# Optimization experiments

Measured on AMD Instinct MI355X. Metric: run time of the kernel, lower is better.

Reference implementation:

```python
import jax, jax.numpy as jnp
import numpy as np

E, MAX_M, K, N = 8, 2048, 2048, 8192

def setup_inputs() -> dict:
    key = jax.random.key(0)
    k1, k2, k3 = jax.random.split(key, 3)
    x_padded = jax.random.normal(k1, (E, MAX_M, K), dtype=jnp.float32)
    stacked_weights = jax.random.normal(k2, (E, N, K), dtype=jnp.float32) * 0.02
    m_sizes = jax.random.randint(k3, (E,), 0, MAX_M, dtype=jnp.int32)
    return {"x_padded": x_padded, "stacked_weights": stacked_weights, "m_sizes": m_sizes}

def reference(x_padded, stacked_weights, m_sizes):
    # valid-token mask per expert: [E, MAX_M]
    mask = (jnp.arange(MAX_M, dtype=jnp.int32)[None, :] < m_sizes[:, None])
    # zero padded rows (pad_expert_inputs fills with zeros)
    x = jnp.where(mask[:, :, None], x_padded, jnp.zeros((), x_padded.dtype))
    # grouped GEMM via batched matmul: [E, M, K] x [E, N, K]^T -> [E, M, N]
    out = jnp.einsum('emk,enk->emn', x, stacked_weights)
    # rows beyond m_sizes[i] are sliced away in the original; mask them to zero
    return jnp.where(mask[:, :, None], out, jnp.zeros((), out.dtype))
```

## Files before the change

kernel.cpp:

```cpp
#include <hip/hip_runtime.h>
#include <hip/hip_bf16.h>


#define NE   8
#define MAXM 2048
#define KD   2048
#define ND   8192

#define BM   256
#define BN   256
#define BK   64
#define NTS  (KD/BK)

typedef __attribute__((ext_vector_type(8))) short          short8;
typedef __attribute__((ext_vector_type(8))) unsigned short us8;
typedef __attribute__((ext_vector_type(4))) float          f32x4;
typedef __attribute__((ext_vector_type(4))) unsigned short us4;

__device__ __forceinline__ unsigned short f2bf(float f) {
    union { float f; unsigned u; } v; v.f = f;
    unsigned u = v.u;
    return (unsigned short)((u + 0x7FFFu + ((u >> 16) & 1u)) >> 16);
}

__device__ __forceinline__ void gload16(const void* g, void* l) {
    __builtin_amdgcn_global_load_lds(
        (const __attribute__((address_space(1))) void*)g,
        (__attribute__((address_space(3))) void*)l, 16, 0, 0);
}

__global__ __launch_bounds__(256) void cvt_kernel(const float* __restrict__ src,
                                                  unsigned short* __restrict__ dst,
                                                  int n8) {
    int i = blockIdx.x * blockDim.x + threadIdx.x;
    int stride = gridDim.x * blockDim.x;
    for (; i < n8; i += stride) {
        const f32x4* s = (const f32x4*)(src + (size_t)i * 8);
        f32x4 a = s[0], b = s[1];
        us8 v = (us8){f2bf(a[0]), f2bf(a[1]), f2bf(a[2]), f2bf(a[3]),
                      f2bf(b[0]), f2bf(b[1]), f2bf(b[2]), f2bf(b[3])};
        *(us8*)(dst + (size_t)i * 8) = v;
    }
}

__global__ __launch_bounds__(256) void cvt_x_kernel(const float* __restrict__ src,
                                                    unsigned short* __restrict__ dst,
                                                    const int* __restrict__ ms) {
    int bid = blockIdx.x;
    int e = bid >> 11, m = bid & 2047;
    if (m >= ms[e]) return;
    const float* s = src + ((size_t)e * MAXM + m) * KD;
    unsigned short* d = dst + ((size_t)e * MAXM + m) * KD;
    int t = threadIdx.x;
    const f32x4* s4 = (const f32x4*)(s + t * 8);
    f32x4 a = s4[0], b = s4[1];
    us8 v = (us8){f2bf(a[0]), f2bf(a[1]), f2bf(a[2]), f2bf(a[3]),
                  f2bf(b[0]), f2bf(b[1]), f2bf(b[2]), f2bf(b[3])};
    *(us8*)(d + t * 8) = v;
}

__global__ __launch_bounds__(512, 2) void ggemm_pers(
    const unsigned short* __restrict__ xb,
    const unsigned short* __restrict__ wb,
    const int*   __restrict__ ms,
    float*       __restrict__ out)
{
    int p   = blockIdx.x;
    int xcd = p & 7;
    int jj  = p >> 3;
    int tid = threadIdx.x;

    __shared__ int s_live[8], s_dead[8], s_cnt[2];
    __shared__ unsigned short Ak[2][2][BM * 32];
    __shared__ unsigned short Bk[2][2][BN * 32];

    if (tid == 0) {
        int nl = 0, nd = 0, cumL = 0, cumD = 0, il = jj, id = jj;
        #pragma unroll
        for (int e = 0; e < NE; ++e) {
            int L = (ms[e] + 255) >> 8;
            int cntL = L << 2, cntD = (8 - L) << 2;
            while (il < cumL + cntL) { int o = il - cumL; s_live[nl++] = (e << 5) | ((o >> 2) << 2) | (o & 3); il += 32; }
            while (id < cumD + cntD) { int o = id - cumD; s_dead[nd++] = (e << 5) | ((L + (o >> 2)) << 2) | (o & 3); id += 32; }
            cumL += cntL; cumD += cntD;
        }
        s_cnt[0] = nl; s_cnt[1] = nd;
    }
    __syncthreads();

    int ndead = s_cnt[1];
    #pragma unroll 1
    for (int d = 0; d < ndead; ++d) {
        int v = s_dead[d]; int e = v >> 5, br = (v >> 2) & 7, bcl = v & 3;
        float* outE = out + (size_t)e * MAXM * ND;
        int row0 = br * BM, col0 = (xcd * 4 + bcl) * BN;
        f32x4 z = (f32x4){0.f, 0.f, 0.f, 0.f};
        #pragma unroll
        for (int q = 0; q < 32; ++q) {
            int i2 = tid + q * 512;
            int rr = i2 >> 6, cc = (i2 & 63) << 2;
            *(f32x4*)(outE + (size_t)(row0 + rr) * ND + col0 + cc) = z;
        }
    }
    int nlive = s_cnt[0];
    if (nlive == 0) return;

    int wid = tid >> 6, lane = tid & 63;
    int wr = wid >> 2, wc = wid & 3;
    int lr = lane & 15, kg = lane >> 4;
    int srow = lane >> 2;
    int ss   = (lane & 3) ^ ((lane >> 3) & 3);

    auto stageA = [&](int b, int kh, const unsigned short* xP, int kt) {
        #pragma unroll
        for (int q = 0; q < 2; ++q) {
            int blk = wid * 2 + q;
            const unsigned short* src =
                xP + (size_t)(blk * 16 + srow) * KD + kt * BK + kh * 32 + ss * 8;
            gload16(src, (char*)&Ak[b][kh][0] + blk * 1024);
        }
    };
    auto stageB = [&](int b, int kh, const unsigned short* wP, int kt) {
        #pragma unroll
        for (int q = 0; q < 2; ++q) {
            int blk = wid * 2 + q;
            const unsigned short* src =
                wP + (size_t)(blk * 16 + srow) * KD + kt * BK + kh * 32 + ss * 8;
            gload16(src, (char*)&Bk[b][kh][0] + blk * 1024);
        }
    };
    auto ldA = [&](short8* a, int b, int kh) {
        #pragma unroll
        for (int mf = 0; mf < 8; ++mf) {
            int row  = wr * 128 + mf * 16 + lr;
            int slot = kg ^ ((row >> 1) & 3);
            a[mf] = *(const short8*)&Ak[b][kh][row * 32 + slot * 8];
        }
    };
    auto ldB4 = [&](short8* bf, int b, int kh) {
        #pragma unroll
        for (int i = 0; i < 4; ++i) {
            int row  = wc * 64 + i * 16 + lr;
            int slot = kg ^ ((row >> 1) & 3);
            bf[i] = *(const short8*)&Bk[b][kh][row * 32 + slot * 8];
        }
    };

    f32x4 acc[8][4];
    #pragma unroll
    for (int mf = 0; mf < 8; ++mf)
        #pragma unroll
        for (int nf = 0; nf < 4; ++nf)
            acc[mf][nf] = (f32x4){0.f, 0.f, 0.f, 0.f};

    const unsigned short *xC, *wC, *xN, *wN;
    float *oC, *oN;
    int msC, r0C, c0C, msN, r0N, c0N;
    {
        int v = s_live[0]; int e = v >> 5, br = (v >> 2) & 7, bcl = v & 3;
        r0C = br * BM; c0C = (xcd * 4 + bcl) * BN; msC = ms[e];
        xC = xb + ((size_t)e * MAXM + r0C) * KD;
        wC = wb + ((size_t)e * ND + c0C) * KD;
        oC = out + (size_t)e * MAXM * ND;
    }
    if (nlive > 1) {
        int v = s_live[1]; int e = v >> 5, br = (v >> 2) & 7, bcl = v & 3;
        r0N = br * BM; c0N = (xcd * 4 + bcl) * BN; msN = ms[e];
        xN = xb + ((size_t)e * MAXM + r0N) * KD;
        wN = wb + ((size_t)e * ND + c0N) * KD;
        oN = out + (size_t)e * MAXM * ND;
    } else { xN = xC; wN = wC; oN = oC; msN = msC; r0N = r0C; c0N = c0C; }

    stageA(0, 0, xC, 0); stageB(0, 0, wC, 0);
    stageA(0, 1, xC, 0); stageB(0, 1, wC, 0);
    stageA(1, 0, xC, 1); stageB(1, 0, wC, 1);
    asm volatile("s_waitcnt vmcnt(8)" ::: "memory");
    __builtin_amdgcn_s_barrier();

    #pragma unroll 1
    for (int s = 0; s < nlive; ++s) {
        bool last  = (s + 1 >= nlive);
        bool alive = (r0C + wr * 128) < msC;

        auto tile = [&](int b, int kt) {
            bool g1 = (kt + 1 < NTS) || (!last);
            bool g2 = (kt + 2 < NTS) || (!last);
            const unsigned short* xS1 = (kt + 1 < NTS) ? xC : xN;
            const unsigned short* wS1 = (kt + 1 < NTS) ? wC : wN;
            int k1 = (kt + 1 < NTS) ? kt + 1 : 0;
            const unsigned short* xS2 = (kt + 2 < NTS) ? xC : xN;
            const unsigned short* wS2 = (kt + 2 < NTS) ? wC : wN;
            int k2 = (kt + 2 < NTS) ? kt + 2 : kt + 2 - NTS;

            short8 a[8], bf[4];
            if (alive) { ldA(a, b, 0); ldB4(bf, b, 0); }
            if (g1) { stageA(b ^ 1, 1, xS1, k1); stageB(b ^ 1, 1, wS1, k1); }
            __builtin_amdgcn_s_barrier();
            __builtin_amdgcn_s_setprio(1);
            if (alive) {
                #pragma unroll
                for (int mf = 0; mf < 8; ++mf)
                    #pragma unroll
                    for (int nf = 0; nf < 4; ++nf)
                        acc[mf][nf] = __builtin_amdgcn_mfma_f32_16x16x32_bf16(a[mf], bf[nf], acc[mf][nf], 0, 0, 0);
            }
            __builtin_amdgcn_s_setprio(0);
            if (g1) { asm volatile("s_waitcnt vmcnt(8)" ::: "memory"); }
            else    { asm volatile("s_waitcnt vmcnt(0)" ::: "memory"); }
            __builtin_amdgcn_s_barrier();
            if (alive) { ldA(a, b, 1); ldB4(bf, b, 1); }
            if (g2) { stageA(b, 0, xS2, k2); stageB(b, 0, wS2, k2); }
            __builtin_amdgcn_s_barrier();
            __builtin_amdgcn_s_setprio(1);
            if (alive) {
                #pragma unroll
                for (int mf = 0; mf < 8; ++mf)
                    #pragma unroll
                    for (int nf = 0; nf < 4; ++nf)
                        acc[mf][nf] = __builtin_amdgcn_mfma_f32_16x16x32_bf16(a[mf], bf[nf], acc[mf][nf], 0, 0, 0);
            }
            __builtin_amdgcn_s_setprio(0);
            if (g2) { asm volatile("s_waitcnt vmcnt(8)" ::: "memory"); }
            else    { asm volatile("s_waitcnt vmcnt(0)" ::: "memory"); }
            __builtin_amdgcn_s_barrier();
        };

        #pragma unroll 1
        for (int kt = 0; kt < NTS; kt += 2) {
            tile(0, kt);
            tile(1, kt + 1);
        }

        #pragma unroll
        for (int mf = 0; mf < 8; ++mf) {
            int rbase = r0C + wr * 128 + mf * 16 + kg * 4;
            #pragma unroll
            for (int nf = 0; nf < 4; ++nf) {
                int gc = c0C + wc * 64 + nf * 16 + lr;
                #pragma unroll
                for (int q = 0; q < 4; ++q) {
                    int gr = rbase + q;
                    float v = (gr < msC) ? acc[mf][nf][q] : 0.f;
                    oC[(size_t)gr * ND + gc] = v;
                    acc[mf][nf][q] = 0.f;
                }
            }
        }

        xC = xN; wC = wN; oC = oN; msC = msN; r0C = r0N; c0C = c0N;
        if (s + 2 < nlive) {
            int v = s_live[s + 2]; int e = v >> 5, br = (v >> 2) & 7, bcl = v & 3;
            r0N = br * BM; c0N = (xcd * 4 + bcl) * BN; msN = ms[e];
            xN = xb + ((size_t)e * MAXM + r0N) * KD;
            wN = wb + ((size_t)e * ND + c0N) * KD;
            oN = out + (size_t)e * MAXM * ND;
        }
    }
}

#define FBM 128
#define FBK 32
#define FTM (MAXM/FBM)
#define FTN (ND/FBM)
#define FNT (KD/FBK)
#define LSTR 40
__global__ __launch_bounds__(256, 2) void ggemm_fused(
    const float* __restrict__ x, const float* __restrict__ w,
    const int* __restrict__ ms, float* __restrict__ out)
{
    int nwg  = gridDim.x;
    int orig = blockIdx.x;
    int cpx  = nwg >> 3;
    int bid  = (orig & 7) * cpx + (orig >> 3);
    int e   = bid / (FTM * FTN);
    int rem = bid % (FTM * FTN);
    int br  = rem % FTM;
    int bc  = rem / FTM;
    int m_size = ms[e];
    int row0 = br * FBM, col0 = bc * FBM;
    float* outE = out + (size_t)e * MAXM * ND;
    int tid = threadIdx.x;

    if (row0 >= m_size) {
        f32x4 z = (f32x4){0.f, 0.f, 0.f, 0.f};
        #pragma unroll
        for (int q = 0; q < 16; ++q) {
            int i2 = tid + q * 256;
            int rr = i2 >> 5, cc = (i2 & 31) << 2;
            *(f32x4*)(outE + (size_t)(row0 + rr) * ND + col0 + cc) = z;
        }
        return;
    }

    const float* xE = x + ((size_t)e * MAXM + row0) * KD;
    const float* wE = w + ((size_t)e * ND   + col0) * KD;

    __shared__ unsigned short As[2][FBM][LSTR];
    __shared__ unsigned short Bs[2][FBM][LSTR];

    int sr  = tid >> 3;
    int sc4 = tid & 7;
    int wid = tid >> 6, lane = tid & 63;
    int wr = wid >> 1, wc = wid & 1;
    int lr = lane & 15, kg = lane >> 4;

    f32x4 acc[4][4];
    #pragma unroll
    for (int m = 0; m < 4; ++m)
        #pragma unroll
        for (int n = 0; n < 4; ++n)
            acc[m][n] = (f32x4){0.f, 0.f, 0.f, 0.f};

    {
        #pragma unroll
        for (int q = 0; q < 4; ++q) {
            int r0 = sr + q * 32;
            f32x4 av = *(const f32x4*)(xE + (size_t)r0 * KD + sc4 * 4);
            f32x4 bv = *(const f32x4*)(wE + (size_t)r0 * KD + sc4 * 4);
            us4 ah = (us4){f2bf(av[0]), f2bf(av[1]), f2bf(av[2]), f2bf(av[3])};
            us4 bh = (us4){f2bf(bv[0]), f2bf(bv[1]), f2bf(bv[2]), f2bf(bv[3])};
            *(us4*)&As[0][r0][sc4 * 4] = ah;
            *(us4*)&Bs[0][r0][sc4 * 4] = bh;
        }
    }
    __syncthreads();

    for (int t = 0; t < FNT; ++t) {
        int cur = t & 1;
        f32x4 av[4], bv[4];
        bool pre = (t + 1 < FNT);
        if (pre) {
            const float* xk = xE + (size_t)(t + 1) * FBK;
            const float* wk = wE + (size_t)(t + 1) * FBK;
            #pragma unroll
            for (int q = 0; q < 4; ++q) {
                int r0 = sr + q * 32;
                av[q] = *(const f32x4*)(xk + (size_t)r0 * KD + sc4 * 4);
                bv[q] = *(const f32x4*)(wk + (size_t)r0 * KD + sc4 * 4);
            }
        }
        short8 a[4], b[4];
        #pragma unroll
        for (int m = 0; m < 4; ++m)
            a[m] = *(const short8*)&As[cur][wr * 64 + m * 16 + lr][kg * 8];
        #pragma unroll
        for (int n = 0; n < 4; ++n)
            b[n] = *(const short8*)&Bs[cur][wc * 64 + n * 16 + lr][kg * 8];
        #pragma unroll
        for (int m = 0; m < 4; ++m)
            #pragma unroll
            for (int n = 0; n < 4; ++n)
                acc[m][n] = __builtin_amdgcn_mfma_f32_16x16x32_bf16(a[m], b[n], acc[m][n], 0, 0, 0);

        if (pre) {
            int nb = cur ^ 1;
            #pragma unroll
            for (int q = 0; q < 4; ++q) {
                int r0 = sr + q * 32;
                us4 ah = (us4){f2bf(av[q][0]), f2bf(av[q][1]), f2bf(av[q][2]), f2bf(av[q][3])};
                us4 bh = (us4){f2bf(bv[q][0]), f2bf(bv[q][1]), f2bf(bv[q][2]), f2bf(bv[q][3])};
                *(us4*)&As[nb][r0][sc4 * 4] = ah;
                *(us4*)&Bs[nb][r0][sc4 * 4] = bh;
            }
        }
        __syncthreads();
    }

    #pragma unroll
    for (int m = 0; m < 4; ++m) {
        int rbase = row0 + wr * 64 + m * 16 + kg * 4;
        #pragma unroll
        for (int n = 0; n < 4; ++n) {
            int gc = col0 + wc * 64 + n * 16 + lr;
            #pragma unroll
            for (int q = 0; q < 4; ++q) {
                int gr = rbase + q;
                float v = (gr < m_size) ? acc[m][n][q] : 0.f;
                outE[(size_t)gr * ND + gc] = v;
            }
        }
    }
}

extern "C" void kernel_launch(void* const* d_in, const int* in_sizes, int n_in,
                              void* d_out, int out_size, void* d_ws, size_t ws_size,
                              hipStream_t stream) {
    const float* x  = (const float*)d_in[0];
    const float* w  = (const float*)d_in[1];
    const int*   ms = (const int*)d_in[2];
    float* out = (float*)d_out;

    const size_t xElems = (size_t)NE * MAXM * KD;
    const size_t wElems = (size_t)NE * ND   * KD;
    const size_t need   = (xElems + wElems) * 2;

    if (ws_size >= need) {
        unsigned short* xb = (unsigned short*)d_ws;
        unsigned short* wb = xb + xElems;
        cvt_x_kernel<<<NE * MAXM, 256, 0, stream>>>(x, xb, ms);
        cvt_kernel<<<2048, 256, 0, stream>>>(w, wb, (int)(wElems / 8));
        ggemm_pers<<<256, 512, 0, stream>>>(xb, wb, ms, out);
    } else {
        ggemm_fused<<<dim3(NE * (MAXM/FBM) * (ND/FBM)), dim3(256), 0, stream>>>(x, w, ms, out);
    }
}
```

Before: 581.2 us.

## Restructure GEMM K-loop pipeline to one barrier per half-tile phase

```diff
diff --git a/kernel.cpp b/kernel.cpp
--- a/kernel.cpp
+++ b/kernel.cpp
@@ -129,22 +129,6 @@
             gload16(src, (char*)&Bk[b][kh][0] + blk * 1024);
         }
     };
-    auto ldA = [&](short8* a, int b, int kh) {
-        #pragma unroll
-        for (int mf = 0; mf < 8; ++mf) {
-            int row  = wr * 128 + mf * 16 + lr;
-            int slot = kg ^ ((row >> 1) & 3);
-            a[mf] = *(const short8*)&Ak[b][kh][row * 32 + slot * 8];
-        }
-    };
-    auto ldB4 = [&](short8* bf, int b, int kh) {
-        #pragma unroll
-        for (int i = 0; i < 4; ++i) {
-            int row  = wc * 64 + i * 16 + lr;
-            int slot = kg ^ ((row >> 1) & 3);
-            bf[i] = *(const short8*)&Bk[b][kh][row * 32 + slot * 8];
-        }
-    };
 
     f32x4 acc[8][4];
     #pragma unroll
@@ -173,62 +157,49 @@
 
     stageA(0, 0, xC, 0); stageB(0, 0, wC, 0);
     stageA(0, 1, xC, 0); stageB(0, 1, wC, 0);
-    stageA(1, 0, xC, 1); stageB(1, 0, wC, 1);
-    asm volatile("s_waitcnt vmcnt(8)" ::: "memory");
-    __builtin_amdgcn_s_barrier();
 
     #pragma unroll 1
     for (int s = 0; s < nlive; ++s) {
         bool last  = (s + 1 >= nlive);
         bool alive = (r0C + wr * 128) < msC;
 
-        auto tile = [&](int b, int kt) {
-            bool g1 = (kt + 1 < NTS) || (!last);
-            bool g2 = (kt + 2 < NTS) || (!last);
-            const unsigned short* xS1 = (kt + 1 < NTS) ? xC : xN;
-            const unsigned short* wS1 = (kt + 1 < NTS) ? wC : wN;
-            int k1 = (kt + 1 < NTS) ? kt + 1 : 0;
-            const unsigned short* xS2 = (kt + 2 < NTS) ? xC : xN;
-            const unsigned short* wS2 = (kt + 2 < NTS) ? wC : wN;
-            int k2 = (kt + 2 < NTS) ? kt + 2 : kt + 2 - NTS;
-
-            short8 a[8], bf[4];
-            if (alive) { ldA(a, b, 0); ldB4(bf, b, 0); }
-            if (g1) { stageA(b ^ 1, 1, xS1, k1); stageB(b ^ 1, 1, wS1, k1); }
+        auto phase = [&](int b, int kh, bool vm4, bool stg,
+                         const unsigned short* xS, const unsigned short* wS, int kts) {
+            if (vm4) { asm volatile("s_waitcnt vmcnt(4)" ::: "memory"); }
+            else     { asm volatile("s_waitcnt vmcnt(0)" ::: "memory"); }
             __builtin_amdgcn_s_barrier();
-            __builtin_amdgcn_s_setprio(1);
+            if (stg) { stageA(b ^ 1, kh, xS, kts); stageB(b ^ 1, kh, wS, kts); }
             if (alive) {
+                short8 a[8], bf[4];
+                #pragma unroll
+                for (int i = 0; i < 4; ++i) {
+                    int row  = wc * 64 + i * 16 + lr;
+                    int slot = kg ^ ((row >> 1) & 3);
+                    bf[i] = *(const short8*)&Bk[b][kh][row * 32 + slot * 8];
+                }
+                #pragma unroll
+                for (int mf = 0; mf < 8; ++mf) {
+                    int row  = wr * 128 + mf * 16 + lr;
+                    int slot = kg ^ ((row >> 1) & 3);
+                    a[mf] = *(const short8*)&Ak[b][kh][row * 32 + slot * 8];
+                }
                 #pragma unroll
                 for (int mf = 0; mf < 8; ++mf)
                     #pragma unroll
                     for (int nf = 0; nf < 4; ++nf)
                         acc[mf][nf] = __builtin_amdgcn_mfma_f32_16x16x32_bf16(a[mf], bf[nf], acc[mf][nf], 0, 0, 0);
             }
-            __builtin_amdgcn_s_setprio(0);
-            if (g1) { asm volatile("s_waitcnt vmcnt(8)" ::: "memory"); }
-            else    { asm volatile("s_waitcnt vmcnt(0)" ::: "memory"); }
-            __builtin_amdgcn_s_barrier();
-            if (alive) { ldA(a, b, 1); ldB4(bf, b, 1); }
-            if (g2) { stageA(b, 0, xS2, k2); stageB(b, 0, wS2, k2); }
-            __builtin_amdgcn_s_barrier();
-            __builtin_amdgcn_s_setprio(1);
-            if (alive) {
-                #pragma unroll
-                for (int mf = 0; mf < 8; ++mf)
-                    #pragma unroll
-                    for (int nf = 0; nf < 4; ++nf)
-                        acc[mf][nf] = __builtin_amdgcn_mfma_f32_16x16x32_bf16(a[mf], bf[nf], acc[mf][nf], 0, 0, 0);
-            }
-            __builtin_amdgcn_s_setprio(0);
-            if (g2) { asm volatile("s_waitcnt vmcnt(8)" ::: "memory"); }
-            else    { asm volatile("s_waitcnt vmcnt(0)" ::: "memory"); }
-            __builtin_amdgcn_s_barrier();
         };
 
         #pragma unroll 1
-        for (int kt = 0; kt < NTS; kt += 2) {
-            tile(0, kt);
-            tile(1, kt + 1);
+        for (int kt = 0; kt < NTS; ++kt) {
+            int b = kt & 1;
+            bool has_next = (kt + 1 < NTS) || (!last);
+            const unsigned short* xS = (kt + 1 < NTS) ? xC : xN;
+            const unsigned short* wS = (kt + 1 < NTS) ? wC : wN;
+            int kts = (kt + 1 < NTS) ? kt + 1 : 0;
+            phase(b, 0, true, has_next, xS, wS, kts);
+            phase(b, 1, has_next, has_next, xS, wS, kts);
         }
 
         #pragma unroll
```

Measured after the change: 663.1 us. 1.14x slower.

## Fuse fp32-to-bf16 weight conversion into persistent GEMM B-tile staging

Applied to the files above, without the earlier changes.

```diff
diff --git a/kernel.cpp b/kernel.cpp
--- a/kernel.cpp
+++ b/kernel.cpp
@@ -27,20 +27,6 @@
     __builtin_amdgcn_global_load_lds(
         (const __attribute__((address_space(1))) void*)g,
         (__attribute__((address_space(3))) void*)l, 16, 0, 0);
-}
-
-__global__ __launch_bounds__(256) void cvt_kernel(const float* __restrict__ src,
-                                                  unsigned short* __restrict__ dst,
-                                                  int n8) {
-    int i = blockIdx.x * blockDim.x + threadIdx.x;
-    int stride = gridDim.x * blockDim.x;
-    for (; i < n8; i += stride) {
-        const f32x4* s = (const f32x4*)(src + (size_t)i * 8);
-        f32x4 a = s[0], b = s[1];
-        us8 v = (us8){f2bf(a[0]), f2bf(a[1]), f2bf(a[2]), f2bf(a[3]),
-                      f2bf(b[0]), f2bf(b[1]), f2bf(b[2]), f2bf(b[3])};
-        *(us8*)(dst + (size_t)i * 8) = v;
-    }
 }
 
 __global__ __launch_bounds__(256) void cvt_x_kernel(const float* __restrict__ src,
@@ -61,7 +47,7 @@
 
 __global__ __launch_bounds__(512, 2) void ggemm_pers(
     const unsigned short* __restrict__ xb,
-    const unsigned short* __restrict__ wb,
+    const float*          __restrict__ w,
     const int*   __restrict__ ms,
     float*       __restrict__ out)
 {
@@ -108,8 +94,10 @@
     int wid = tid >> 6, lane = tid & 63;
     int wr = wid >> 2, wc = wid & 3;
     int lr = lane & 15, kg = lane >> 4;
-    int srow = lane >> 2;
-    int ss   = (lane & 3) ^ ((lane >> 3) & 3);
+    int srow  = lane >> 2;
+    int ss    = (lane & 3) ^ ((lane >> 3) & 3);
+    int sslot = lane & 3;
+    int ssw   = sslot ^ ((lane >> 3) & 3);
 
     auto stageA = [&](int b, int kh, const unsigned short* xP, int kt) {
         #pragma unroll
@@ -120,13 +108,23 @@
             gload16(src, (char*)&Ak[b][kh][0] + blk * 1024);
         }
     };
-    auto stageB = [&](int b, int kh, const unsigned short* wP, int kt) {
+    auto loadB = [&](f32x4* bl, const float* wP, int kt, int kh) {
         #pragma unroll
         for (int q = 0; q < 2; ++q) {
             int blk = wid * 2 + q;
-            const unsigned short* src =
-                wP + (size_t)(blk * 16 + srow) * KD + kt * BK + kh * 32 + ss * 8;
-            gload16(src, (char*)&Bk[b][kh][0] + blk * 1024);
+            const float* src = wP + (size_t)(blk * 16 + srow) * KD + kt * BK + kh * 32 + sslot * 8;
+            bl[2 * q]     = *(const f32x4*)(src);
+            bl[2 * q + 1] = *(const f32x4*)(src + 4);
+        }
+    };
+    auto writeB = [&](int b, int kh, const f32x4* bl) {
+        #pragma unroll
+        for (int q = 0; q < 2; ++q) {
+            int blk = wid * 2 + q;
+            f32x4 lo = bl[2 * q], hi = bl[2 * q + 1];
+            us8 v = (us8){f2bf(lo[0]), f2bf(lo[1]), f2bf(lo[2]), f2bf(lo[3]),
+                          f2bf(hi[0]), f2bf(hi[1]), f2bf(hi[2]), f2bf(hi[3])};
+            *(us8*)((char*)&Bk[b][kh][0] + blk * 1024 + srow * 64 + ssw * 16) = v;
         }
     };
     auto ldA = [&](short8* a, int b, int kh) {
@@ -153,28 +151,32 @@
         for (int nf = 0; nf < 4; ++nf)
             acc[mf][nf] = (f32x4){0.f, 0.f, 0.f, 0.f};
 
-    const unsigned short *xC, *wC, *xN, *wN;
+    f32x4 bl0[4], bl1[4];
+
+    const unsigned short *xC, *xN;
+    const float *wC, *wN;
     float *oC, *oN;
     int msC, r0C, c0C, msN, r0N, c0N;
     {
         int v = s_live[0]; int e = v >> 5, br = (v >> 2) & 7, bcl = v & 3;
         r0C = br * BM; c0C = (xcd * 4 + bcl) * BN; msC = ms[e];
         xC = xb + ((size_t)e * MAXM + r0C) * KD;
-        wC = wb + ((size_t)e * ND + c0C) * KD;
+        wC = w  + ((size_t)e * ND + c0C) * KD;
         oC = out + (size_t)e * MAXM * ND;
     }
     if (nlive > 1) {
         int v = s_live[1]; int e = v >> 5, br = (v >> 2) & 7, bcl = v & 3;
         r0N = br * BM; c0N = (xcd * 4 + bcl) * BN; msN = ms[e];
         xN = xb + ((size_t)e * MAXM + r0N) * KD;
-        wN = wb + ((size_t)e * ND + c0N) * KD;
+        wN = w  + ((size_t)e * ND + c0N) * KD;
         oN = out + (size_t)e * MAXM * ND;
     } else { xN = xC; wN = wC; oN = oC; msN = msC; r0N = r0C; c0N = c0C; }
 
-    stageA(0, 0, xC, 0); stageB(0, 0, wC, 0);
-    stageA(0, 1, xC, 0); stageB(0, 1, wC, 0);
-    stageA(1, 0, xC, 1); stageB(1, 0, wC, 1);
-    asm volatile("s_waitcnt vmcnt(8)" ::: "memory");
+    stageA(0, 0, xC, 0); stageA(0, 1, xC, 0); stageA(1, 0, xC, 1);
+    loadB(bl0, wC, 0, 0); writeB(0, 0, bl0);
+    loadB(bl0, wC, 0, 1); writeB(0, 1, bl0);
+    loadB(bl1, wC, 1, 1);
+    asm volatile("s_waitcnt vmcnt(4) lgkmcnt(0)" ::: "memory");
     __builtin_amdgcn_s_barrier();
 
     #pragma unroll 1
@@ -182,19 +184,23 @@
         bool last  = (s + 1 >= nlive);
         bool alive = (r0C + wr * 128) < msC;
 
-        auto tile = [&](int b, int kt) {
+        #pragma unroll 1
+        for (int kt = 0; kt < NTS; ++kt) {
+            int b = kt & 1;
             bool g1 = (kt + 1 < NTS) || (!last);
             bool g2 = (kt + 2 < NTS) || (!last);
             const unsigned short* xS1 = (kt + 1 < NTS) ? xC : xN;
-            const unsigned short* wS1 = (kt + 1 < NTS) ? wC : wN;
+            const float*          wF1 = (kt + 1 < NTS) ? wC : wN;
             int k1 = (kt + 1 < NTS) ? kt + 1 : 0;
             const unsigned short* xS2 = (kt + 2 < NTS) ? xC : xN;
-            const unsigned short* wS2 = (kt + 2 < NTS) ? wC : wN;
+            const float*          wF2 = (kt + 2 < NTS) ? wC : wN;
             int k2 = (kt + 2 < NTS) ? kt + 2 : kt + 2 - NTS;
 
             short8 a[8], bf[4];
-            if (alive) { ldA(a, b, 0); ldB4(bf, b, 0); }
-            if (g1) { stageA(b ^ 1, 1, xS1, k1); stageB(b ^ 1, 1, wS1, k1); }
+
+            if (g1) stageA(b ^ 1, 1, xS1, k1);
+            if (g1) loadB(bl0, wF1, k1, 0);
+            if (alive) { ldB4(bf, b, 0); ldA(a, b, 0); }
             __builtin_amdgcn_s_barrier();
             __builtin_amdgcn_s_setprio(1);
             if (alive) {
@@ -205,11 +211,14 @@
                         acc[mf][nf] = __builtin_amdgcn_mfma_f32_16x16x32_bf16(a[mf], bf[nf], acc[mf][nf], 0, 0, 0);
             }
             __builtin_amdgcn_s_setprio(0);
-            if (g1) { asm volatile("s_waitcnt vmcnt(8)" ::: "memory"); }
-            else    { asm volatile("s_waitcnt vmcnt(0)" ::: "memory"); }
+            if (g1) writeB(b ^ 1, 1, bl1);
+            if (g1) { asm volatile("s_waitcnt vmcnt(6) lgkmcnt(0)" ::: "memory"); }
+            else    { asm volatile("s_waitcnt vmcnt(0) lgkmcnt(0)" ::: "memory"); }
             __builtin_amdgcn_s_barrier();
-            if (alive) { ldA(a, b, 1); ldB4(bf, b, 1); }
-            if (g2) { stageA(b, 0, xS2, k2); stageB(b, 0, wS2, k2); }
+
+            if (g2) stageA(b, 0, xS2, k2);
+            if (g2) loadB(bl1, wF2, k2, 1);
+            if (alive) { ldB4(bf, b, 1); ldA(a, b, 1); }
             __builtin_amdgcn_s_barrier();
             __builtin_amdgcn_s_setprio(1);
             if (alive) {
@@ -220,15 +229,10 @@
                         acc[mf][nf] = __builtin_amdgcn_mfma_f32_16x16x32_bf16(a[mf], bf[nf], acc[mf][nf], 0, 0, 0);
             }
             __builtin_amdgcn_s_setprio(0);
-            if (g2) { asm volatile("s_waitcnt vmcnt(8)" ::: "memory"); }
-            else    { asm volatile("s_waitcnt vmcnt(0)" ::: "memory"); }
+            if (g1) writeB(b ^ 1, 0, bl0);
+            if (g2) { asm volatile("s_waitcnt vmcnt(6) lgkmcnt(0)" ::: "memory"); }
+            else    { asm volatile("s_waitcnt vmcnt(0) lgkmcnt(0)" ::: "memory"); }
             __builtin_amdgcn_s_barrier();
-        };
-
-        #pragma unroll 1
-        for (int kt = 0; kt < NTS; kt += 2) {
-            tile(0, kt);
-            tile(1, kt + 1);
         }
 
         #pragma unroll
@@ -252,7 +256,7 @@
             int v = s_live[s + 2]; int e = v >> 5, br = (v >> 2) & 7, bcl = v & 3;
             r0N = br * BM; c0N = (xcd * 4 + bcl) * BN; msN = ms[e];
             xN = xb + ((size_t)e * MAXM + r0N) * KD;
-            wN = wb + ((size_t)e * ND + c0N) * KD;
+            wN = w  + ((size_t)e * ND + c0N) * KD;
             oN = out + (size_t)e * MAXM * ND;
         }
     }
@@ -391,15 +395,12 @@
     float* out = (float*)d_out;
 
     const size_t xElems = (size_t)NE * MAXM * KD;
-    const size_t wElems = (size_t)NE * ND   * KD;
-    const size_t need   = (xElems + wElems) * 2;
+    const size_t need   = xElems * 2;
 
     if (ws_size >= need) {
         unsigned short* xb = (unsigned short*)d_ws;
-        unsigned short* wb = xb + xElems;
         cvt_x_kernel<<<NE * MAXM, 256, 0, stream>>>(x, xb, ms);
-        cvt_kernel<<<2048, 256, 0, stream>>>(w, wb, (int)(wElems / 8));
-        ggemm_pers<<<256, 512, 0, stream>>>(xb, wb, ms, out);
+        ggemm_pers<<<256, 512, 0, stream>>>(xb, w, ms, out);
     } else {
         ggemm_fused<<<dim3(NE * (MAXM/FBM) * (ND/FBM)), dim3(256), 0, stream>>>(x, w, ms, out);
     }
```

Result: slower. 625.2 us (+7.6%).
